# Kernel tuning notes

Measured on AMD Instinct MI355X. Metric: run time of the kernel, lower is better.

Reference implementation:

```python
import jax, jax.numpy as jnp
import numpy as np

N_WIN = 7    # n_win hardcoded in AR_Attention
TOPK = 4     # topk routing windows
HEADS = 8    # num_heads


def setup_inputs() -> dict:
    key = jax.random.key(0)
    ks = jax.random.split(key, 6)
    B, H, W, C = 4, 56, 56, 256
    s = 0.02
    x = jax.random.normal(ks[0], (B, H, W, C), jnp.float32)
    Wqkv = jax.random.normal(ks[1], (C, 3 * C), jnp.float32) * s  # Linear(dim, 3*dim) (qk_dim=dim)
    bqkv = jnp.zeros((3 * C,), jnp.float32)
    Wo = jax.random.normal(ks[2], (C, C), jnp.float32) * s        # output projection Linear(dim, dim)
    bo = jnp.zeros((C,), jnp.float32)
    lepe_w = jax.random.normal(ks[3], (5, 5, 1, C), jnp.float32) * s  # 5x5 depthwise conv (side_dwconv=5)
    lepe_b = jnp.zeros((C,), jnp.float32)
    return {"x": x, "Wqkv": Wqkv, "bqkv": bqkv, "Wo": Wo, "bo": bo,
            "lepe_w": lepe_w, "lepe_b": lepe_b}


def reference(x, Wqkv, bqkv, Wo, bo, lepe_w, lepe_b):
    B, H, W, C = x.shape
    nw = N_WIN
    h, w = H // nw, W // nw           # region size (8x8)
    p2 = nw * nw                      # number of regions (49)
    hd = C // HEADS                   # head dim
    scale = float(C) ** -0.5          # qk_scale = qk_dim ** -0.5 (qk_dim = dim)

    # region partition: [B,H,W,C] -> [B,p2,h,w,C]
    xr = x.reshape(B, nw, h, nw, w, C).transpose(0, 1, 3, 2, 4, 5).reshape(B, p2, h, w, C)

    qkv = xr @ Wqkv + bqkv            # [B,p2,h,w,3C]
    q, kv = qkv[..., :C], qkv[..., C:]

    q_pix = q.reshape(B, p2, h * w, C)
    kv_pix = kv.reshape(B, p2, h * w, 2 * C)   # kv_downsample_mode='identity'

    # region-level queries/keys via per-window mean pooling
    q_win = q.mean((2, 3))                     # [B,p2,C]
    k_win = kv[..., :C].mean((2, 3))           # [B,p2,C]

    # LEPE: 5x5 depthwise conv on v over the full image grid
    v_img = kv[..., C:].reshape(B, nw, nw, h, w, C).transpose(0, 1, 3, 2, 4, 5).reshape(B, H, W, C)
    lepe = jax.lax.conv_general_dilated(
        v_img, lepe_w, (1, 1), 'SAME',
        dimension_numbers=('NHWC', 'HWIO', 'NHWC'),
        feature_group_count=C) + lepe_b

    # top-k window routing (param_routing=False, hard routing, mul_weight='none')
    r_logit = jnp.einsum('bpc,bqc->bpq', q_win * scale, k_win)  # [B,p2,p2]
    _, r_idx = jax.lax.top_k(r_logit, TOPK)                     # [B,p2,TOPK]

    # gather selected kv windows: [B,p2,TOPK,h*w,2C]
    kv_sel = jax.vmap(lambda kvp, i: kvp[i])(kv_pix, r_idx)

    k_sel = kv_sel[..., :C].reshape(B, p2, TOPK * h * w, HEADS, hd)
    v_sel = kv_sel[..., C:].reshape(B, p2, TOPK * h * w, HEADS, hd)
    qh = q_pix.reshape(B, p2, h * w, HEADS, hd)

    attn = jnp.einsum('bpqnd,bpknd->bpnqk', qh * scale, k_sel)  # [B,p2,heads,hw,TOPK*hw]
    attn = jax.nn.softmax(attn, axis=-1)
    out = jnp.einsum('bpnqk,bpknd->bpqnd', attn, v_sel).reshape(B, p2, h, w, C)

    # windows back to image grid
    out = out.reshape(B, nw, nw, h, w, C).transpose(0, 1, 3, 2, 4, 5).reshape(B, H, W, C)
    out = out + lepe
    return out @ Wo + bo
```

## Files before the change

kernel.cpp:

```cpp
#include <hip/hip_runtime.h>
#include <hip/hip_bf16.h>

#define NPIX 12544

typedef short bf16x8 __attribute__((ext_vector_type(8)));
typedef short bf16x4 __attribute__((ext_vector_type(4)));
typedef float f32x4  __attribute__((ext_vector_type(4)));

__device__ __forceinline__ float bf2f(unsigned short u) {
    unsigned int x = ((unsigned int)u) << 16;
    float f; __builtin_memcpy(&f, &x, sizeof(f)); return f;
}
__device__ __forceinline__ unsigned short f2bf(float f) {
    __hip_bfloat16 h = __float2bfloat16(f);
    unsigned short u; __builtin_memcpy(&u, &h, 2); return u;
}
__device__ __forceinline__ void load_lds16(const unsigned short* g, unsigned short* l) {
    __builtin_amdgcn_global_load_lds(
        (const __attribute__((address_space(1))) unsigned int*)g,
        (__attribute__((address_space(3))) unsigned int*)l,
        16, 0, 0);
}
__device__ __forceinline__ unsigned ldsoff(const void* p) {
    return (unsigned)(unsigned long long)(const __attribute__((address_space(3))) char*)p;
}
template<int OFF>
__device__ __forceinline__ bf16x4 tr16(unsigned addr) {
    bf16x4 d;
    asm volatile("ds_read_b64_tr_b16 %0, %1 offset:%c2"
                 : "=v"(d) : "v"(addr), "i"(OFF));
    return d;
}

__global__ __launch_bounds__(256) void k_prep(
    const float* __restrict__ X, unsigned short* __restrict__ Xb,
    float* __restrict__ xmean,
    const float* __restrict__ Wqkv, const float* __restrict__ Wo,
    unsigned short* __restrict__ Wtq, unsigned short* __restrict__ Wto)
{
    __shared__ __align__(16) unsigned char sm[64 * 65 * 4];
    const int t = threadIdx.x;
    const int blk = blockIdx.x;
    if (blk < 392) {
        float* part = (float*)sm;
        const int w = blk >> 1, hc = blk & 1;
        const int b = w / 49, p = w % 49;
        const int wi = p / 7, wj = p % 7;
        const int ch0 = hc * 128;
        const int ps = t >> 5, cg = t & 31;
        float4 s = {0.f, 0.f, 0.f, 0.f};
        #pragma unroll
        for (int i = 0; i < 8; i++) {
            int pp = ps * 8 + i;
            int y = wi * 8 + (pp >> 3), x = wj * 8 + (pp & 7);
            int idx = (((b * 56) + y) * 56 + x) * 256 + ch0 + cg * 4;
            float4 v = *reinterpret_cast<const float4*>(X + idx);
            s.x += v.x; s.y += v.y; s.z += v.z; s.w += v.w;
            ushort4 o = { f2bf(v.x), f2bf(v.y), f2bf(v.z), f2bf(v.w) };
            *reinterpret_cast<ushort4*>(Xb + idx) = o;
        }
        *reinterpret_cast<float4*>(part + t * 4) = *reinterpret_cast<float4*>(&s);
        __syncthreads();
        if (t < 32) {
            float4 m = {0.f, 0.f, 0.f, 0.f};
            #pragma unroll
            for (int ps2 = 0; ps2 < 8; ps2++) {
                float4 v = *reinterpret_cast<float4*>(part + (ps2 * 32 + t) * 4);
                m.x += v.x; m.y += v.y; m.z += v.z; m.w += v.w;
            }
            m.x *= (1.f / 64.f); m.y *= (1.f / 64.f);
            m.z *= (1.f / 64.f); m.w *= (1.f / 64.f);
            *reinterpret_cast<float4*>(xmean + w * 256 + ch0 + t * 4) = m;
        }
    } else {
        float* tile = (float*)sm;
        int tb = blk - 392;
        const float* Wsrc; unsigned short* Wdst; int N, kt, nt;
        if (tb < 48) { Wsrc = Wqkv; Wdst = Wtq; N = 768; kt = tb / 12; nt = tb % 12; }
        else { tb -= 48; Wsrc = Wo; Wdst = Wto; N = 256; kt = tb / 4; nt = tb % 4; }
        const int k0 = kt * 64, n0 = nt * 64;
        const int r0 = t >> 6, c = t & 63;
        #pragma unroll
        for (int i = 0; i < 16; i++) {
            int r = i * 4 + r0;
            tile[r * 65 + c] = Wsrc[(size_t)(k0 + r) * N + n0 + c];
        }
        __syncthreads();
        #pragma unroll
        for (int i = 0; i < 16; i++) {
            int n = i * 4 + r0;
            Wdst[(size_t)(n0 + n) * 256 + k0 + c] = f2bf(tile[c * 65 + n]);
        }
    }
}

__global__ __launch_bounds__(256) void k_main1(
    const unsigned short* __restrict__ A,
    const unsigned short* __restrict__ Bt,
    const float* __restrict__ bias,
    unsigned short* __restrict__ O,
    const float* __restrict__ xmean,
    const float* __restrict__ Wqkv,
    float* __restrict__ qwin, float* __restrict__ kwin)
{
    __shared__ __align__(16) unsigned char sm1[32768];
    const int t = threadIdx.x;
    const int blk = blockIdx.x;
    if (blk < 588) {
        unsigned short* As = (unsigned short*)sm1;
        unsigned short* Bs = (unsigned short*)(sm1 + 16384);
        const int m0 = (blk % 98) * 128, n0 = (blk / 98) * 128;
        const int wave = t >> 6, lane = t & 63, quad = lane >> 4, lo = lane & 15;
        const int wm = wave & 1, wn = wave >> 1;
        const int sr = wave * 16 + (lane >> 2);
        const int sc = lane & 3;
        f32x4 acc[4][4];
        #pragma unroll
        for (int i = 0; i < 4; i++)
            #pragma unroll
            for (int j = 0; j < 4; j++) acc[i][j] = (f32x4){0.f, 0.f, 0.f, 0.f};

        auto stage = [&](int it) {
            int kt = it * 32;
            unsigned short* Ad = As + (it & 1) * 4096;
            unsigned short* Bd = Bs + (it & 1) * 4096;
            #pragma unroll
            for (int j = 0; j < 2; j++) {
                int row = j * 64 + sr;
                int e = sc ^ ((row >> 1) & 3);
                load_lds16(A  + (size_t)(m0 + row) * 256 + kt + e * 8, &Ad[row * 32 + sc * 8]);
                load_lds16(Bt + (size_t)(n0 + row) * 256 + kt + e * 8, &Bd[row * 32 + sc * 8]);
            }
        };
        stage(0);
        for (int it = 0; it < 8; ++it) {
            if (it < 7) {
                stage(it + 1);
                asm volatile("s_waitcnt vmcnt(4)" ::: "memory");
            } else {
                asm volatile("s_waitcnt vmcnt(0)" ::: "memory");
            }
            __builtin_amdgcn_s_barrier();
            const unsigned short* Ac = As + (it & 1) * 4096;
            const unsigned short* Bc = Bs + (it & 1) * 4096;
            bf16x8 af[4], bfr[4];
            #pragma unroll
            for (int mt = 0; mt < 4; mt++) {
                int row = wm * 64 + mt * 16 + lo;
                int c = quad ^ ((row >> 1) & 3);
                af[mt] = *reinterpret_cast<const bf16x8*>(&Ac[row * 32 + c * 8]);
            }
            #pragma unroll
            for (int nt = 0; nt < 4; nt++) {
                int col = wn * 64 + nt * 16 + lo;
                int c = quad ^ ((col >> 1) & 3);
                bfr[nt] = *reinterpret_cast<const bf16x8*>(&Bc[col * 32 + c * 8]);
            }
            #pragma unroll
            for (int mt = 0; mt < 4; mt++)
                #pragma unroll
                for (int nt = 0; nt < 4; nt++)
                    acc[mt][nt] = __builtin_amdgcn_mfma_f32_16x16x32_bf16(
                        af[mt], bfr[nt], acc[mt][nt], 0, 0, 0);
            __builtin_amdgcn_s_barrier();
        }
        float bv[4];
        #pragma unroll
        for (int nt = 0; nt < 4; nt++) bv[nt] = bias[n0 + wn * 64 + nt * 16 + lo];
        #pragma unroll
        for (int mt = 0; mt < 4; mt++)
            #pragma unroll
            for (int nt = 0; nt < 4; nt++) {
                int n = n0 + wn * 64 + nt * 16 + lo;
                #pragma unroll
                for (int r = 0; r < 4; r++) {
                    int m = m0 + wm * 64 + mt * 16 + quad * 4 + r;
                    O[m * 768 + n] = f2bf(acc[mt][nt][r] + bv[nt]);
                }
            }
    } else {
        float* xs = (float*)sm1;
        const int u = blk - 588;
        const int bp = u % 196;
        const int half = u / 196;
        const int c = t;
        xs[c] = xmean[bp * 256 + c];
        __syncthreads();
        const int col = half * 256 + c;
        float a = 0.f;
        for (int k = 0; k < 256; k++) a += xs[k] * Wqkv[k * 768 + col];
        float* outp = half ? kwin : qwin;
        outp[bp * 256 + c] = a + bias[col];
    }
}

__global__ __launch_bounds__(256) void k_main2(
    const float* __restrict__ qwin, const float* __restrict__ kwin,
    int* __restrict__ ridx,
    const unsigned short* __restrict__ QKV,
    const float* __restrict__ lw, const float* __restrict__ lb,
    unsigned short* __restrict__ Olepe)
{
    __shared__ __align__(16) unsigned char sm2[25600];
    const int t = threadIdx.x;
    const int blk = blockIdx.x;
    if (blk < 196) {
        float* part = (float*)sm2;
        float* lg   = (float*)(sm2 + 49 * 4 * 4);
        const int b = blk / 49, p = blk % 49;
        if (t < 196) {
            int d = t >> 2, pr = t & 3;
            const float* qp = &qwin[(b * 49 + p) * 256];
            const float* kp = &kwin[(b * 49 + d) * 256];
            float a = 0.f;
            for (int ch = pr * 64; ch < pr * 64 + 64; ch++) a += qp[ch] * kp[ch];
            part[d * 4 + pr] = a;
        }
        __syncthreads();
        if (t < 49) lg[t] = part[t * 4 + 0] + part[t * 4 + 1] + part[t * 4 + 2] + part[t * 4 + 3];
        __syncthreads();
        if (t == 0) {
            unsigned long long used = 0ull;
            for (int sel = 0; sel < 4; sel++) {
                float best = -1e30f; int bi = 0;
                for (int qq = 0; qq < 49; qq++)
                    if (!((used >> qq) & 1ull) && lg[qq] > best) { best = lg[qq]; bi = qq; }
                used |= (1ull << bi);
                ridx[blk * 4 + sel] = bi;
            }
        }
    } else {
        float* lws = (float*)sm2;
        #pragma unroll
        for (int i = 0; i < 25; i++) lws[i * 256 + t] = lw[i * 256 + t];

        const int pl = t & 7;
        const int cg = t >> 3;
        const int c0 = cg * 8;
        const int gid = (blk - 196) * 8 + pl;
        const int b = gid / 3136, rem = gid % 3136;
        const int y = rem / 56, x = rem % 56;
        __syncthreads();

        float acc[8];
        {
            float4 b0 = *reinterpret_cast<const float4*>(lb + c0);
            float4 b1 = *reinterpret_cast<const float4*>(lb + c0 + 4);
            acc[0] = b0.x; acc[1] = b0.y; acc[2] = b0.z; acc[3] = b0.w;
            acc[4] = b1.x; acc[5] = b1.y; acc[6] = b1.z; acc[7] = b1.w;
        }
        #pragma unroll
        for (int ky = 0; ky < 5; ky++) {
            int yy = y + ky - 2;
            if (yy < 0 || yy >= 56) continue;
            #pragma unroll
            for (int kx = 0; kx < 5; kx++) {
                int xx = x + kx - 2;
                if (xx < 0 || xx >= 56) continue;
                bf16x8 v = *reinterpret_cast<const bf16x8*>(
                    QKV + (((b * 56) + yy) * 56 + xx) * 768 + 512 + c0);
                const float* wrow = &lws[(ky * 5 + kx) * 256 + c0];
                float4 w0 = *reinterpret_cast<const float4*>(wrow);
                float4 w1 = *reinterpret_cast<const float4*>(wrow + 4);
                acc[0] += bf2f((unsigned short)v[0]) * w0.x;
                acc[1] += bf2f((unsigned short)v[1]) * w0.y;
                acc[2] += bf2f((unsigned short)v[2]) * w0.z;
                acc[3] += bf2f((unsigned short)v[3]) * w0.w;
                acc[4] += bf2f((unsigned short)v[4]) * w1.x;
                acc[5] += bf2f((unsigned short)v[5]) * w1.y;
                acc[6] += bf2f((unsigned short)v[6]) * w1.z;
                acc[7] += bf2f((unsigned short)v[7]) * w1.w;
            }
        }
        bf16x8 o;
        #pragma unroll
        for (int j = 0; j < 8; j++) o[j] = (short)f2bf(acc[j]);
        *reinterpret_cast<bf16x8*>(Olepe + (size_t)gid * 256 + c0) = o;
    }
}

__global__ __launch_bounds__(256) void k_attn(
    const unsigned short* __restrict__ QKV,
    const int* __restrict__ ridx,
    const unsigned short* __restrict__ Olepe,
    unsigned short* __restrict__ Osum)
{
    __shared__ __align__(16) unsigned char smem[40960];
    unsigned short* Vs  = (unsigned short*)smem;
    unsigned short* Ks  = (unsigned short*)(smem + 16384);
    unsigned short* PST = (unsigned short*)(smem + 32768);

    const int p = blockIdx.x, head = blockIdx.y, b = blockIdx.z;
    const int t = threadIdx.x;
    const int wi = p / 7, wj = p % 7;
    const int wave = t >> 6, lane = t & 63, quad = lane >> 4, lo = lane & 15;
    const int pix4 = t >> 2, c4 = t & 3;

    const int q  = wave * 16 + lo;
    const int qy = wi * 8 + (q >> 3), qx = wj * 8 + (q & 7);

    bf16x8 af = *reinterpret_cast<const bf16x8*>(
        QKV + (size_t)(((b * 56) + qy) * 56 + qx) * 768 + head * 32 + quad * 8);

    {
        const int4 rs = *reinterpret_cast<const int4*>(&ridx[(b * 49 + p) * 4]);
        const int sels[4] = { rs.x, rs.y, rs.z, rs.w };
        #pragma unroll
        for (int pass = 0; pass < 4; pass++) {
            int sel = sels[pass];
            int si = sel / 7, sj = sel % 7;
            int y = si * 8 + (pix4 >> 3), x = sj * 8 + (pix4 & 7);
            const unsigned short* base = QKV + (((b * 56) + y) * 56 + x) * 768 + 256 + head * 32;
            bf16x8 kv = *reinterpret_cast<const bf16x8*>(base + c4 * 8);
            bf16x8 vv = *reinterpret_cast<const bf16x8*>(base + 256 + c4 * 8);
            int krow = pass * 64 + pix4;
            *reinterpret_cast<bf16x8*>(&Ks[krow * 32 + c4 * 8]) = kv;
            *reinterpret_cast<bf16x8*>(
                &Vs[(krow >> 2) * 128 + (c4 >> 1) * 64 + (krow & 3) * 16 + (c4 & 1) * 8]) = vv;
        }
    }
    __syncthreads();

    const f32x4 z = (f32x4){0.f, 0.f, 0.f, 0.f};

    float M[4] = {-1e30f, -1e30f, -1e30f, -1e30f};
    #pragma unroll 4
    for (int nt = 0; nt < 16; nt++) {
        bf16x8 bfr = *reinterpret_cast<const bf16x8*>(&Ks[(nt * 16 + lo) * 32 + quad * 8]);
        f32x4 s = __builtin_amdgcn_mfma_f32_16x16x32_bf16(af, bfr, z, 0, 0, 0);
        #pragma unroll
        for (int r = 0; r < 4; r++) M[r] = fmaxf(M[r], s[r] * 0.0625f);
    }
    #pragma unroll
    for (int d = 1; d < 16; d <<= 1)
        #pragma unroll
        for (int r = 0; r < 4; r++) M[r] = fmaxf(M[r], __shfl_xor(M[r], d));

    unsigned short* myP = PST + wave * 1024;
    const unsigned pbase = ldsoff(myP) + quad * 256 + lo * 8;
    const unsigned vbase = ldsoff(Vs)  + quad * 512 + lo * 8;
    float l[4] = {0.f, 0.f, 0.f, 0.f};
    f32x4 o0 = z, o1 = z;
    for (int c = 0; c < 4; c++) {
        f32x4 s[4];
        #pragma unroll
        for (int td = 0; td < 4; td++) {
            bf16x8 kf = *reinterpret_cast<const bf16x8*>(
                &Ks[((4 * c + td) * 16 + lo) * 32 + quad * 8]);
            s[td] = __builtin_amdgcn_mfma_f32_16x16x32_bf16(af, kf, z, 0, 0, 0);
        }
        #pragma unroll
        for (int td = 0; td < 4; td++) {
            float e[4];
            #pragma unroll
            for (int r = 0; r < 4; r++) {
                e[r] = __expf(s[td][r] * 0.0625f - M[r]);
                l[r] += e[r];
            }
            ushort4 pk = { f2bf(e[0]), f2bf(e[1]), f2bf(e[2]), f2bf(e[3]) };
            *reinterpret_cast<ushort4*>(&myP[(td * 16 + lo) * 16 + quad * 4]) = pk;
        }
        asm volatile("s_waitcnt lgkmcnt(0)" ::: "memory");
        __builtin_amdgcn_sched_barrier(0);

        const unsigned vb0a = vbase + (2 * c) * 2048;
        const unsigned vb1a = vbase + (2 * c + 1) * 2048;
        bf16x4 ra0 = tr16<0>(pbase);
        bf16x4 ra1 = tr16<128>(pbase);
        bf16x4 rb0 = tr16<1024>(pbase);
        bf16x4 rb1 = tr16<1152>(pbase);
        bf16x4 w00 = tr16<0>(vb0a),  w01 = tr16<256>(vb0a);
        bf16x4 w10 = tr16<128>(vb0a), w11 = tr16<384>(vb0a);
        bf16x4 x00 = tr16<0>(vb1a),  x01 = tr16<256>(vb1a);
        bf16x4 x10 = tr16<128>(vb1a), x11 = tr16<384>(vb1a);
        asm volatile("s_waitcnt lgkmcnt(0)" ::: "memory");
        __builtin_amdgcn_sched_barrier(0);
        bf16x8 pa, pb, va0, va1, vc0, vc1;
        #pragma unroll
        for (int j = 0; j < 4; j++) {
            pa[j]  = ra0[j]; pa[4 + j]  = ra1[j];
            pb[j]  = rb0[j]; pb[4 + j]  = rb1[j];
            va0[j] = w00[j]; va0[4 + j] = w01[j];
            va1[j] = w10[j]; va1[4 + j] = w11[j];
            vc0[j] = x00[j]; vc0[4 + j] = x01[j];
            vc1[j] = x10[j]; vc1[4 + j] = x11[j];
        }
        o0 = __builtin_amdgcn_mfma_f32_16x16x32_bf16(pa, va0, o0, 0, 0, 0);
        o1 = __builtin_amdgcn_mfma_f32_16x16x32_bf16(pa, va1, o1, 0, 0, 0);
        o0 = __builtin_amdgcn_mfma_f32_16x16x32_bf16(pb, vc0, o0, 0, 0, 0);
        o1 = __builtin_amdgcn_mfma_f32_16x16x32_bf16(pb, vc1, o1, 0, 0, 0);
    }
    #pragma unroll
    for (int d = 1; d < 16; d <<= 1)
        #pragma unroll
        for (int r = 0; r < 4; r++) l[r] += __shfl_xor(l[r], d);

    {
        float i0 = 1.f / l[0], i1 = 1.f / l[1], i2 = 1.f / l[2], i3 = 1.f / l[3];
        ushort4 p0 = { f2bf(o0[0] * i0), f2bf(o0[1] * i1),
                       f2bf(o0[2] * i2), f2bf(o0[3] * i3) };
        ushort4 p1 = { f2bf(o1[0] * i0), f2bf(o1[1] * i1),
                       f2bf(o1[2] * i2), f2bf(o1[3] * i3) };
        *reinterpret_cast<ushort4*>(&myP[lo * 16 + quad * 4]) = p0;
        *reinterpret_cast<ushort4*>(&myP[(16 + lo) * 16 + quad * 4]) = p1;
    }
    const unsigned oaddr = ldsoff(myP) + quad * 256 + lo * 8;
    asm volatile("s_waitcnt lgkmcnt(0)" ::: "memory");
    __builtin_amdgcn_sched_barrier(0);
    bf16x4 e0 = tr16<0>(oaddr);
    bf16x4 e1 = tr16<128>(oaddr);
    asm volatile("s_waitcnt lgkmcnt(0)" ::: "memory");
    __builtin_amdgcn_sched_barrier(0);
    {
        size_t gbase = (size_t)(((b * 56) + qy) * 56 + qx) * 256 + head * 32 + quad * 8;
        bf16x8 lp = *reinterpret_cast<const bf16x8*>(Olepe + gbase);
        bf16x8 oo;
        #pragma unroll
        for (int j = 0; j < 4; j++) {
            oo[j]     = (short)f2bf(bf2f((unsigned short)e0[j]) + bf2f((unsigned short)lp[j]));
            oo[4 + j] = (short)f2bf(bf2f((unsigned short)e1[j]) + bf2f((unsigned short)lp[4 + j]));
        }
        *reinterpret_cast<bf16x8*>(Osum + gbase) = oo;
    }
}

__global__ __launch_bounds__(256) void k_proj(
    const unsigned short* __restrict__ A,
    const unsigned short* __restrict__ Bt,
    const float* __restrict__ bias,
    float* __restrict__ O)
{
    __shared__ __align__(16) unsigned short As[2 * 64 * 32];
    __shared__ __align__(16) unsigned short Bs[2 * 64 * 32];
    const int t = threadIdx.x;
    const int m0 = blockIdx.x * 64, n0 = blockIdx.y * 64;
    const int wave = t >> 6, lane = t & 63, quad = lane >> 4, lo = lane & 15;
    const int sr = wave * 16 + (lane >> 2);
    const int sc = lane & 3;
    f32x4 acc[4];
    #pragma unroll
    for (int j = 0; j < 4; j++) acc[j] = (f32x4){0.f, 0.f, 0.f, 0.f};

    auto stage = [&](int it) {
        int kt = it * 32;
        unsigned short* Ad = As + (it & 1) * 2048;
        unsigned short* Bd = Bs + (it & 1) * 2048;
        int e = sc ^ ((sr >> 1) & 3);
        load_lds16(A  + (size_t)(m0 + sr) * 256 + kt + e * 8, &Ad[sr * 32 + sc * 8]);
        load_lds16(Bt + (size_t)(n0 + sr) * 256 + kt + e * 8, &Bd[sr * 32 + sc * 8]);
    };
    stage(0);
    for (int it = 0; it < 8; ++it) {
        if (it < 7) {
            stage(it + 1);
            asm volatile("s_waitcnt vmcnt(2)" ::: "memory");
        } else {
            asm volatile("s_waitcnt vmcnt(0)" ::: "memory");
        }
        __builtin_amdgcn_s_barrier();
        const unsigned short* Ac = As + (it & 1) * 2048;
        const unsigned short* Bc = Bs + (it & 1) * 2048;
        bf16x8 af;
        {
            int row = wave * 16 + lo;
            int c = quad ^ ((row >> 1) & 3);
            af = *reinterpret_cast<const bf16x8*>(&Ac[row * 32 + c * 8]);
        }
        bf16x8 bfr[4];
        #pragma unroll
        for (int nt = 0; nt < 4; nt++) {
            int col = nt * 16 + lo;
            int c = quad ^ ((col >> 1) & 3);
            bfr[nt] = *reinterpret_cast<const bf16x8*>(&Bc[col * 32 + c * 8]);
        }
        #pragma unroll
        for (int nt = 0; nt < 4; nt++)
            acc[nt] = __builtin_amdgcn_mfma_f32_16x16x32_bf16(af, bfr[nt], acc[nt], 0, 0, 0);
        __builtin_amdgcn_s_barrier();
    }
    float bv[4];
    #pragma unroll
    for (int nt = 0; nt < 4; nt++) bv[nt] = bias[n0 + nt * 16 + lo];
    #pragma unroll
    for (int nt = 0; nt < 4; nt++) {
        int n = n0 + nt * 16 + lo;
        #pragma unroll
        for (int r = 0; r < 4; r++) {
            int m = m0 + wave * 16 + quad * 4 + r;
            O[m * 256 + n] = acc[nt][r] + bv[nt];
        }
    }
}

extern "C" void kernel_launch(void* const* d_in, const int* in_sizes, int n_in,
                              void* d_out, int out_size, void* d_ws, size_t ws_size,
                              hipStream_t stream)
{
    const float* x    = (const float*)d_in[0];
    const float* Wqkv = (const float*)d_in[1];
    const float* bqkv = (const float*)d_in[2];
    const float* Wo   = (const float*)d_in[3];
    const float* bo   = (const float*)d_in[4];
    const float* lw   = (const float*)d_in[5];
    const float* lb   = (const float*)d_in[6];
    float* out = (float*)d_out;

    char* ws = (char*)d_ws;
    size_t off = 0;
    unsigned short* qkv   = (unsigned short*)(ws + off); off += (size_t)NPIX * 768 * 2;
    unsigned short* xb    = (unsigned short*)(ws + off); off += (size_t)NPIX * 256 * 2;
    unsigned short* Wtq   = (unsigned short*)(ws + off); off += 768 * 256 * 2;
    unsigned short* Wto   = (unsigned short*)(ws + off); off += 256 * 256 * 2;
    unsigned short* Osum  = (unsigned short*)(ws + off); off += (size_t)NPIX * 256 * 2;
    unsigned short* Olepe = (unsigned short*)(ws + off); off += (size_t)NPIX * 256 * 2;
    float* xmean = (float*)(ws + off); off += 196 * 256 * 4;
    float* qwin  = (float*)(ws + off); off += 196 * 256 * 4;
    float* kwin  = (float*)(ws + off); off += 196 * 256 * 4;
    int*   ridx  = (int*)(ws + off);   off += 196 * 4 * 4;

    k_prep <<<dim3(456),      256, 0, stream>>>(x, xb, xmean, Wqkv, Wo, Wtq, Wto);
    k_main1<<<dim3(980),      256, 0, stream>>>(xb, Wtq, bqkv, qkv, xmean, Wqkv, qwin, kwin);
    k_main2<<<dim3(1764),     256, 0, stream>>>(qwin, kwin, ridx, qkv, lw, lb, Olepe);
    k_attn <<<dim3(49, 8, 4), 256, 0, stream>>>(qkv, ridx, Olepe, Osum);
    k_proj <<<dim3(196, 4),   256, 0, stream>>>(Osum, Wto, bo, out);
}
```

Measured before the change: 150.7 us.

## Split routing into own kernel, co-schedule attention with LEPE conv, fold add into projection

```diff
diff --git a/kernel.cpp b/kernel.cpp
--- a/kernel.cpp
+++ b/kernel.cpp
@@ -194,50 +194,191 @@
     }
 }
 
-__global__ __launch_bounds__(256) void k_main2(
+__global__ __launch_bounds__(256) void k_route(
     const float* __restrict__ qwin, const float* __restrict__ kwin,
-    int* __restrict__ ridx,
+    int* __restrict__ ridx)
+{
+    __shared__ __align__(16) unsigned char sm2[1024];
+    const int t = threadIdx.x;
+    const int blk = blockIdx.x;
+    float* part = (float*)sm2;
+    float* lg   = (float*)(sm2 + 49 * 4 * 4);
+    const int b = blk / 49, p = blk % 49;
+    if (t < 196) {
+        int d = t >> 2, pr = t & 3;
+        const float* qp = &qwin[(b * 49 + p) * 256];
+        const float* kp = &kwin[(b * 49 + d) * 256];
+        float a = 0.f;
+        for (int ch = pr * 64; ch < pr * 64 + 64; ch++) a += qp[ch] * kp[ch];
+        part[d * 4 + pr] = a;
+    }
+    __syncthreads();
+    if (t < 49) lg[t] = part[t * 4 + 0] + part[t * 4 + 1] + part[t * 4 + 2] + part[t * 4 + 3];
+    __syncthreads();
+    if (t == 0) {
+        unsigned long long used = 0ull;
+        for (int sel = 0; sel < 4; sel++) {
+            float best = -1e30f; int bi = 0;
+            for (int qq = 0; qq < 49; qq++)
+                if (!((used >> qq) & 1ull) && lg[qq] > best) { best = lg[qq]; bi = qq; }
+            used |= (1ull << bi);
+            ridx[blk * 4 + sel] = bi;
+        }
+    }
+}
+
+__global__ __launch_bounds__(256) void k_attn(
     const unsigned short* __restrict__ QKV,
+    const int* __restrict__ ridx,
     const float* __restrict__ lw, const float* __restrict__ lb,
+    unsigned short* __restrict__ Osum,
     unsigned short* __restrict__ Olepe)
 {
-    __shared__ __align__(16) unsigned char sm2[25600];
+    __shared__ __align__(16) unsigned char smem[40960];
     const int t = threadIdx.x;
     const int blk = blockIdx.x;
-    if (blk < 196) {
-        float* part = (float*)sm2;
-        float* lg   = (float*)(sm2 + 49 * 4 * 4);
-        const int b = blk / 49, p = blk % 49;
-        if (t < 196) {
-            int d = t >> 2, pr = t & 3;
-            const float* qp = &qwin[(b * 49 + p) * 256];
-            const float* kp = &kwin[(b * 49 + d) * 256];
-            float a = 0.f;
-            for (int ch = pr * 64; ch < pr * 64 + 64; ch++) a += qp[ch] * kp[ch];
-            part[d * 4 + pr] = a;
+
+    if (blk < 1568) {
+        unsigned short* Vs  = (unsigned short*)smem;
+        unsigned short* Ks  = (unsigned short*)(smem + 16384);
+        unsigned short* PST = (unsigned short*)(smem + 32768);
+
+        const int p = blk % 49, head = (blk / 49) % 8, b = blk / 392;
+        const int wi = p / 7, wj = p % 7;
+        const int wave = t >> 6, lane = t & 63, quad = lane >> 4, lo = lane & 15;
+        const int pix4 = t >> 2, c4 = t & 3;
+
+        const int q  = wave * 16 + lo;
+        const int qy = wi * 8 + (q >> 3), qx = wj * 8 + (q & 7);
+
+        bf16x8 af = *reinterpret_cast<const bf16x8*>(
+            QKV + (size_t)(((b * 56) + qy) * 56 + qx) * 768 + head * 32 + quad * 8);
+
+        {
+            const int4 rs = *reinterpret_cast<const int4*>(&ridx[(b * 49 + p) * 4]);
+            const int sels[4] = { rs.x, rs.y, rs.z, rs.w };
+            #pragma unroll
+            for (int pass = 0; pass < 4; pass++) {
+                int sel = sels[pass];
+                int si = sel / 7, sj = sel % 7;
+                int y = si * 8 + (pix4 >> 3), x = sj * 8 + (pix4 & 7);
+                const unsigned short* base = QKV + (((b * 56) + y) * 56 + x) * 768 + 256 + head * 32;
+                bf16x8 kv = *reinterpret_cast<const bf16x8*>(base + c4 * 8);
+                bf16x8 vv = *reinterpret_cast<const bf16x8*>(base + 256 + c4 * 8);
+                int krow = pass * 64 + pix4;
+                *reinterpret_cast<bf16x8*>(&Ks[krow * 32 + c4 * 8]) = kv;
+                *reinterpret_cast<bf16x8*>(
+                    &Vs[(krow >> 2) * 128 + (c4 >> 1) * 64 + (krow & 3) * 16 + (c4 & 1) * 8]) = vv;
+            }
         }
         __syncthreads();
-        if (t < 49) lg[t] = part[t * 4 + 0] + part[t * 4 + 1] + part[t * 4 + 2] + part[t * 4 + 3];
-        __syncthreads();
-        if (t == 0) {
-            unsigned long long used = 0ull;
-            for (int sel = 0; sel < 4; sel++) {
-                float best = -1e30f; int bi = 0;
-                for (int qq = 0; qq < 49; qq++)
-                    if (!((used >> qq) & 1ull) && lg[qq] > best) { best = lg[qq]; bi = qq; }
-                used |= (1ull << bi);
-                ridx[blk * 4 + sel] = bi;
-            }
+
+        const f32x4 z = (f32x4){0.f, 0.f, 0.f, 0.f};
+
+        float M[4] = {-1e30f, -1e30f, -1e30f, -1e30f};
+        #pragma unroll 4
+        for (int nt = 0; nt < 16; nt++) {
+            bf16x8 bfr = *reinterpret_cast<const bf16x8*>(&Ks[(nt * 16 + lo) * 32 + quad * 8]);
+            f32x4 s = __builtin_amdgcn_mfma_f32_16x16x32_bf16(af, bfr, z, 0, 0, 0);
+            #pragma unroll
+            for (int r = 0; r < 4; r++) M[r] = fmaxf(M[r], s[r] * 0.0625f);
+        }
+        #pragma unroll
+        for (int d = 1; d < 16; d <<= 1)
+            #pragma unroll
+            for (int r = 0; r < 4; r++) M[r] = fmaxf(M[r], __shfl_xor(M[r], d));
+
+        unsigned short* myP = PST + wave * 1024;
+        const unsigned pbase = ldsoff(myP) + quad * 256 + lo * 8;
+        const unsigned vbase = ldsoff(Vs)  + quad * 512 + lo * 8;
+        float l[4] = {0.f, 0.f, 0.f, 0.f};
+        f32x4 o0 = z, o1 = z;
+        for (int c = 0; c < 4; c++) {
+            f32x4 s[4];
+            #pragma unroll
+            for (int td = 0; td < 4; td++) {
+                bf16x8 kf = *reinterpret_cast<const bf16x8*>(
+                    &Ks[((4 * c + td) * 16 + lo) * 32 + quad * 8]);
+                s[td] = __builtin_amdgcn_mfma_f32_16x16x32_bf16(af, kf, z, 0, 0, 0);
+            }
+            #pragma unroll
+            for (int td = 0; td < 4; td++) {
+                float e[4];
+                #pragma unroll
+                for (int r = 0; r < 4; r++) {
+                    e[r] = __expf(s[td][r] * 0.0625f - M[r]);
+                    l[r] += e[r];
+                }
+                ushort4 pk = { f2bf(e[0]), f2bf(e[1]), f2bf(e[2]), f2bf(e[3]) };
+                *reinterpret_cast<ushort4*>(&myP[(td * 16 + lo) * 16 + quad * 4]) = pk;
+            }
+            asm volatile("s_waitcnt lgkmcnt(0)" ::: "memory");
+            __builtin_amdgcn_sched_barrier(0);
+
+            const unsigned vb0a = vbase + (2 * c) * 2048;
+            const unsigned vb1a = vbase + (2 * c + 1) * 2048;
+            bf16x4 ra0 = tr16<0>(pbase);
+            bf16x4 ra1 = tr16<128>(pbase);
+            bf16x4 rb0 = tr16<1024>(pbase);
+            bf16x4 rb1 = tr16<1152>(pbase);
+            bf16x4 w00 = tr16<0>(vb0a),  w01 = tr16<256>(vb0a);
+            bf16x4 w10 = tr16<128>(vb0a), w11 = tr16<384>(vb0a);
+            bf16x4 x00 = tr16<0>(vb1a),  x01 = tr16<256>(vb1a);
+            bf16x4 x10 = tr16<128>(vb1a), x11 = tr16<384>(vb1a);
+            asm volatile("s_waitcnt lgkmcnt(0)" ::: "memory");
+            __builtin_amdgcn_sched_barrier(0);
+            bf16x8 pa, pb, va0, va1, vc0, vc1;
+            #pragma unroll
+            for (int j = 0; j < 4; j++) {
+                pa[j]  = ra0[j]; pa[4 + j]  = ra1[j];
+                pb[j]  = rb0[j]; pb[4 + j]  = rb1[j];
+                va0[j] = w00[j]; va0[4 + j] = w01[j];
+                va1[j] = w10[j]; va1[4 + j] = w11[j];
+                vc0[j] = x00[j]; vc0[4 + j] = x01[j];
+                vc1[j] = x10[j]; vc1[4 + j] = x11[j];
+            }
+            o0 = __builtin_amdgcn_mfma_f32_16x16x32_bf16(pa, va0, o0, 0, 0, 0);
+            o1 = __builtin_amdgcn_mfma_f32_16x16x32_bf16(pa, va1, o1, 0, 0, 0);
+            o0 = __builtin_amdgcn_mfma_f32_16x16x32_bf16(pb, vc0, o0, 0, 0, 0);
+            o1 = __builtin_amdgcn_mfma_f32_16x16x32_bf16(pb, vc1, o1, 0, 0, 0);
+        }
+        #pragma unroll
+        for (int d = 1; d < 16; d <<= 1)
+            #pragma unroll
+            for (int r = 0; r < 4; r++) l[r] += __shfl_xor(l[r], d);
+
+        {
+            float i0 = 1.f / l[0], i1 = 1.f / l[1], i2 = 1.f / l[2], i3 = 1.f / l[3];
+            ushort4 p0 = { f2bf(o0[0] * i0), f2bf(o0[1] * i1),
+                           f2bf(o0[2] * i2), f2bf(o0[3] * i3) };
+            ushort4 p1 = { f2bf(o1[0] * i0), f2bf(o1[1] * i1),
+                           f2bf(o1[2] * i2), f2bf(o1[3] * i3) };
+            *reinterpret_cast<ushort4*>(&myP[lo * 16 + quad * 4]) = p0;
+            *reinterpret_cast<ushort4*>(&myP[(16 + lo) * 16 + quad * 4]) = p1;
+        }
+        const unsigned oaddr = ldsoff(myP) + quad * 256 + lo * 8;
+        asm volatile("s_waitcnt lgkmcnt(0)" ::: "memory");
+        __builtin_amdgcn_sched_barrier(0);
+        bf16x4 e0 = tr16<0>(oaddr);
+        bf16x4 e1 = tr16<128>(oaddr);
+        asm volatile("s_waitcnt lgkmcnt(0)" ::: "memory");
+        __builtin_amdgcn_sched_barrier(0);
+        {
+            size_t gbase = (size_t)(((b * 56) + qy) * 56 + qx) * 256 + head * 32 + quad * 8;
+            bf16x8 oo;
+            #pragma unroll
+            for (int j = 0; j < 4; j++) { oo[j] = e0[j]; oo[4 + j] = e1[j]; }
+            *reinterpret_cast<bf16x8*>(Osum + gbase) = oo;
         }
     } else {
-        float* lws = (float*)sm2;
+        float* lws = (float*)smem;
         #pragma unroll
         for (int i = 0; i < 25; i++) lws[i * 256 + t] = lw[i * 256 + t];
 
         const int pl = t & 7;
         const int cg = t >> 3;
         const int c0 = cg * 8;
-        const int gid = (blk - 196) * 8 + pl;
+        const int gid = (blk - 1568) * 8 + pl;
         const int b = gid / 3136, rem = gid % 3136;
         const int y = rem / 56, x = rem % 56;
         __syncthreads();
@@ -279,158 +420,15 @@
     }
 }
 
-__global__ __launch_bounds__(256) void k_attn(
-    const unsigned short* __restrict__ QKV,
-    const int* __restrict__ ridx,
-    const unsigned short* __restrict__ Olepe,
-    unsigned short* __restrict__ Osum)
-{
-    __shared__ __align__(16) unsigned char smem[40960];
-    unsigned short* Vs  = (unsigned short*)smem;
-    unsigned short* Ks  = (unsigned short*)(smem + 16384);
-    unsigned short* PST = (unsigned short*)(smem + 32768);
-
-    const int p = blockIdx.x, head = blockIdx.y, b = blockIdx.z;
-    const int t = threadIdx.x;
-    const int wi = p / 7, wj = p % 7;
-    const int wave = t >> 6, lane = t & 63, quad = lane >> 4, lo = lane & 15;
-    const int pix4 = t >> 2, c4 = t & 3;
-
-    const int q  = wave * 16 + lo;
-    const int qy = wi * 8 + (q >> 3), qx = wj * 8 + (q & 7);
-
-    bf16x8 af = *reinterpret_cast<const bf16x8*>(
-        QKV + (size_t)(((b * 56) + qy) * 56 + qx) * 768 + head * 32 + quad * 8);
-
-    {
-        const int4 rs = *reinterpret_cast<const int4*>(&ridx[(b * 49 + p) * 4]);
-        const int sels[4] = { rs.x, rs.y, rs.z, rs.w };
-        #pragma unroll
-        for (int pass = 0; pass < 4; pass++) {
-            int sel = sels[pass];
-            int si = sel / 7, sj = sel % 7;
-            int y = si * 8 + (pix4 >> 3), x = sj * 8 + (pix4 & 7);
-            const unsigned short* base = QKV + (((b * 56) + y) * 56 + x) * 768 + 256 + head * 32;
-            bf16x8 kv = *reinterpret_cast<const bf16x8*>(base + c4 * 8);
-            bf16x8 vv = *reinterpret_cast<const bf16x8*>(base + 256 + c4 * 8);
-            int krow = pass * 64 + pix4;
-            *reinterpret_cast<bf16x8*>(&Ks[krow * 32 + c4 * 8]) = kv;
-            *reinterpret_cast<bf16x8*>(
-                &Vs[(krow >> 2) * 128 + (c4 >> 1) * 64 + (krow & 3) * 16 + (c4 & 1) * 8]) = vv;
-        }
-    }
-    __syncthreads();
-
-    const f32x4 z = (f32x4){0.f, 0.f, 0.f, 0.f};
-
-    float M[4] = {-1e30f, -1e30f, -1e30f, -1e30f};
-    #pragma unroll 4
-    for (int nt = 0; nt < 16; nt++) {
-        bf16x8 bfr = *reinterpret_cast<const bf16x8*>(&Ks[(nt * 16 + lo) * 32 + quad * 8]);
-        f32x4 s = __builtin_amdgcn_mfma_f32_16x16x32_bf16(af, bfr, z, 0, 0, 0);
-        #pragma unroll
-        for (int r = 0; r < 4; r++) M[r] = fmaxf(M[r], s[r] * 0.0625f);
-    }
-    #pragma unroll
-    for (int d = 1; d < 16; d <<= 1)
-        #pragma unroll
-        for (int r = 0; r < 4; r++) M[r] = fmaxf(M[r], __shfl_xor(M[r], d));
-
-    unsigned short* myP = PST + wave * 1024;
-    const unsigned pbase = ldsoff(myP) + quad * 256 + lo * 8;
-    const unsigned vbase = ldsoff(Vs)  + quad * 512 + lo * 8;
-    float l[4] = {0.f, 0.f, 0.f, 0.f};
-    f32x4 o0 = z, o1 = z;
-    for (int c = 0; c < 4; c++) {
-        f32x4 s[4];
-        #pragma unroll
-        for (int td = 0; td < 4; td++) {
-            bf16x8 kf = *reinterpret_cast<const bf16x8*>(
-                &Ks[((4 * c + td) * 16 + lo) * 32 + quad * 8]);
-            s[td] = __builtin_amdgcn_mfma_f32_16x16x32_bf16(af, kf, z, 0, 0, 0);
-        }
-        #pragma unroll
-        for (int td = 0; td < 4; td++) {
-            float e[4];
-            #pragma unroll
-            for (int r = 0; r < 4; r++) {
-                e[r] = __expf(s[td][r] * 0.0625f - M[r]);
-                l[r] += e[r];
-            }
-            ushort4 pk = { f2bf(e[0]), f2bf(e[1]), f2bf(e[2]), f2bf(e[3]) };
-            *reinterpret_cast<ushort4*>(&myP[(td * 16 + lo) * 16 + quad * 4]) = pk;
-        }
-        asm volatile("s_waitcnt lgkmcnt(0)" ::: "memory");
-        __builtin_amdgcn_sched_barrier(0);
-
-        const unsigned vb0a = vbase + (2 * c) * 2048;
-        const unsigned vb1a = vbase + (2 * c + 1) * 2048;
-        bf16x4 ra0 = tr16<0>(pbase);
-        bf16x4 ra1 = tr16<128>(pbase);
-        bf16x4 rb0 = tr16<1024>(pbase);
-        bf16x4 rb1 = tr16<1152>(pbase);
-        bf16x4 w00 = tr16<0>(vb0a),  w01 = tr16<256>(vb0a);
-        bf16x4 w10 = tr16<128>(vb0a), w11 = tr16<384>(vb0a);
-        bf16x4 x00 = tr16<0>(vb1a),  x01 = tr16<256>(vb1a);
-        bf16x4 x10 = tr16<128>(vb1a), x11 = tr16<384>(vb1a);
-        asm volatile("s_waitcnt lgkmcnt(0)" ::: "memory");
-        __builtin_amdgcn_sched_barrier(0);
-        bf16x8 pa, pb, va0, va1, vc0, vc1;
-        #pragma unroll
-        for (int j = 0; j < 4; j++) {
-            pa[j]  = ra0[j]; pa[4 + j]  = ra1[j];
-            pb[j]  = rb0[j]; pb[4 + j]  = rb1[j];
-            va0[j] = w00[j]; va0[4 + j] = w01[j];
-            va1[j] = w10[j]; va1[4 + j] = w11[j];
-            vc0[j] = x00[j]; vc0[4 + j] = x01[j];
-            vc1[j] = x10[j]; vc1[4 + j] = x11[j];
-        }
-        o0 = __builtin_amdgcn_mfma_f32_16x16x32_bf16(pa, va0, o0, 0, 0, 0);
-        o1 = __builtin_amdgcn_mfma_f32_16x16x32_bf16(pa, va1, o1, 0, 0, 0);
-        o0 = __builtin_amdgcn_mfma_f32_16x16x32_bf16(pb, vc0, o0, 0, 0, 0);
-        o1 = __builtin_amdgcn_mfma_f32_16x16x32_bf16(pb, vc1, o1, 0, 0, 0);
-    }
-    #pragma unroll
-    for (int d = 1; d < 16; d <<= 1)
-        #pragma unroll
-        for (int r = 0; r < 4; r++) l[r] += __shfl_xor(l[r], d);
-
-    {
-        float i0 = 1.f / l[0], i1 = 1.f / l[1], i2 = 1.f / l[2], i3 = 1.f / l[3];
-        ushort4 p0 = { f2bf(o0[0] * i0), f2bf(o0[1] * i1),
-                       f2bf(o0[2] * i2), f2bf(o0[3] * i3) };
-        ushort4 p1 = { f2bf(o1[0] * i0), f2bf(o1[1] * i1),
-                       f2bf(o1[2] * i2), f2bf(o1[3] * i3) };
-        *reinterpret_cast<ushort4*>(&myP[lo * 16 + quad * 4]) = p0;
-        *reinterpret_cast<ushort4*>(&myP[(16 + lo) * 16 + quad * 4]) = p1;
-    }
-    const unsigned oaddr = ldsoff(myP) + quad * 256 + lo * 8;
-    asm volatile("s_waitcnt lgkmcnt(0)" ::: "memory");
-    __builtin_amdgcn_sched_barrier(0);
-    bf16x4 e0 = tr16<0>(oaddr);
-    bf16x4 e1 = tr16<128>(oaddr);
-    asm volatile("s_waitcnt lgkmcnt(0)" ::: "memory");
-    __builtin_amdgcn_sched_barrier(0);
-    {
-        size_t gbase = (size_t)(((b * 56) + qy) * 56 + qx) * 256 + head * 32 + quad * 8;
-        bf16x8 lp = *reinterpret_cast<const bf16x8*>(Olepe + gbase);
-        bf16x8 oo;
-        #pragma unroll
-        for (int j = 0; j < 4; j++) {
-            oo[j]     = (short)f2bf(bf2f((unsigned short)e0[j]) + bf2f((unsigned short)lp[j]));
-            oo[4 + j] = (short)f2bf(bf2f((unsigned short)e1[j]) + bf2f((unsigned short)lp[4 + j]));
-        }
-        *reinterpret_cast<bf16x8*>(Osum + gbase) = oo;
-    }
-}
-
 __global__ __launch_bounds__(256) void k_proj(
-    const unsigned short* __restrict__ A,
+    const unsigned short* __restrict__ S,
+    const unsigned short* __restrict__ L,
     const unsigned short* __restrict__ Bt,
     const float* __restrict__ bias,
     float* __restrict__ O)
 {
     __shared__ __align__(16) unsigned short As[2 * 64 * 32];
+    __shared__ __align__(16) unsigned short Al[2 * 64 * 32];
     __shared__ __align__(16) unsigned short Bs[2 * 64 * 32];
     const int t = threadIdx.x;
     const int m0 = blockIdx.x * 64, n0 = blockIdx.y * 64;
@@ -444,27 +442,31 @@
     auto stage = [&](int it) {
         int kt = it * 32;
         unsigned short* Ad = As + (it & 1) * 2048;
+        unsigned short* Ld = Al + (it & 1) * 2048;
         unsigned short* Bd = Bs + (it & 1) * 2048;
         int e = sc ^ ((sr >> 1) & 3);
-        load_lds16(A  + (size_t)(m0 + sr) * 256 + kt + e * 8, &Ad[sr * 32 + sc * 8]);
+        load_lds16(S  + (size_t)(m0 + sr) * 256 + kt + e * 8, &Ad[sr * 32 + sc * 8]);
+        load_lds16(L  + (size_t)(m0 + sr) * 256 + kt + e * 8, &Ld[sr * 32 + sc * 8]);
         load_lds16(Bt + (size_t)(n0 + sr) * 256 + kt + e * 8, &Bd[sr * 32 + sc * 8]);
     };
     stage(0);
     for (int it = 0; it < 8; ++it) {
         if (it < 7) {
             stage(it + 1);
-            asm volatile("s_waitcnt vmcnt(2)" ::: "memory");
+            asm volatile("s_waitcnt vmcnt(3)" ::: "memory");
         } else {
             asm volatile("s_waitcnt vmcnt(0)" ::: "memory");
         }
         __builtin_amdgcn_s_barrier();
         const unsigned short* Ac = As + (it & 1) * 2048;
+        const unsigned short* Lc = Al + (it & 1) * 2048;
         const unsigned short* Bc = Bs + (it & 1) * 2048;
-        bf16x8 af;
+        bf16x8 af_s, af_l;
         {
             int row = wave * 16 + lo;
             int c = quad ^ ((row >> 1) & 3);
-            af = *reinterpret_cast<const bf16x8*>(&Ac[row * 32 + c * 8]);
+            af_s = *reinterpret_cast<const bf16x8*>(&Ac[row * 32 + c * 8]);
+            af_l = *reinterpret_cast<const bf16x8*>(&Lc[row * 32 + c * 8]);
         }
         bf16x8 bfr[4];
         #pragma unroll
@@ -474,8 +476,10 @@
             bfr[nt] = *reinterpret_cast<const bf16x8*>(&Bc[col * 32 + c * 8]);
         }
         #pragma unroll
-        for (int nt = 0; nt < 4; nt++)
-            acc[nt] = __builtin_amdgcn_mfma_f32_16x16x32_bf16(af, bfr[nt], acc[nt], 0, 0, 0);
+        for (int nt = 0; nt < 4; nt++) {
+            acc[nt] = __builtin_amdgcn_mfma_f32_16x16x32_bf16(af_s, bfr[nt], acc[nt], 0, 0, 0);
+            acc[nt] = __builtin_amdgcn_mfma_f32_16x16x32_bf16(af_l, bfr[nt], acc[nt], 0, 0, 0);
+        }
         __builtin_amdgcn_s_barrier();
     }
     float bv[4];
@@ -520,7 +524,7 @@
 
     k_prep <<<dim3(456),      256, 0, stream>>>(x, xb, xmean, Wqkv, Wo, Wtq, Wto);
     k_main1<<<dim3(980),      256, 0, stream>>>(xb, Wtq, bqkv, qkv, xmean, Wqkv, qwin, kwin);
-    k_main2<<<dim3(1764),     256, 0, stream>>>(qwin, kwin, ridx, qkv, lw, lb, Olepe);
-    k_attn <<<dim3(49, 8, 4), 256, 0, stream>>>(qkv, ridx, Olepe, Osum);
-    k_proj <<<dim3(196, 4),   256, 0, stream>>>(Osum, Wto, bo, out);
-}
+    k_route<<<dim3(196),      256, 0, stream>>>(qwin, kwin, ridx);
+    k_attn <<<dim3(3136),     256, 0, stream>>>(qkv, ridx, lw, lb, Osum, Olepe);
+    k_proj <<<dim3(196, 4),   256, 0, stream>>>(Osum, Olepe, Wto, bo, out);
+}
```

After: 161.9 us. 7.4% more time.
